# Performance work log

Measured on AMD Instinct MI355X. Metric: run time of the kernel, lower is better.

Reference implementation:

```python
import jax, jax.numpy as jnp
import numpy as np

B, S, H, I, G = 4, 2048, 2048, 8192, 128


def _onebit_quant(w, group_size):
    # Group-wise 1-bit (sign) quantization along the input dim with per-group
    # abs-mean scale, as in BitNet-style OneBitLinear.
    out_f, in_f = w.shape
    wg = w.reshape(out_f, in_f // group_size, group_size)
    scale = jnp.mean(jnp.abs(wg), axis=-1, keepdims=True)  # [out, n_groups, 1]
    wq = jnp.sign(wg) * scale
    return wq.reshape(out_f, in_f)


def setup_inputs() -> dict:
    key = jax.random.key(0)
    k1, k2, k3, k4 = jax.random.split(key, 4)
    return {
        "x": jax.random.normal(k1, (B, S, H), dtype=jnp.float32),
        "w_gate": jax.random.normal(k2, (I, H), dtype=jnp.float32) * 0.02,
        "w_up": jax.random.normal(k3, (I, H), dtype=jnp.float32) * 0.02,
        "w_down": jax.random.normal(k4, (H, I), dtype=jnp.float32) * 0.02,
        "group_size": G,
    }


def reference(x, w_gate, w_up, w_down, group_size):
    wg_q = _onebit_quant(w_gate, group_size)   # [I, H]
    wu_q = _onebit_quant(w_up, group_size)     # [I, H]
    wd_q = _onebit_quant(w_down, group_size)   # [H, I]
    gate = jnp.einsum('bsh,ih->bsi', x, wg_q)  # [B, S, I]
    up = jnp.einsum('bsh,ih->bsi', x, wu_q)    # [B, S, I]
    h = jax.nn.silu(gate) * up                 # [B, S, I]
    return jnp.einsum('bsi,hi->bsh', h, wd_q)  # [B, S, H]
```

## Files before the change

kernel.cpp:

```cpp
#include <hip/hip_runtime.h>
#include <hip/hip_bf16.h>
#include <cstdint>
#include <cstddef>

using bf16 = __hip_bfloat16;

typedef __attribute__((ext_vector_type(8))) short short8;
typedef __attribute__((ext_vector_type(4))) float f32x4;
typedef __attribute__((ext_vector_type(4))) unsigned short us4;

static constexpr int Bb = 4, Ss = 2048, Hh = 2048, Ii = 8192, Gg = 128;
static constexpr int Mm = Bb * Ss;

#define MEMFENCE() asm volatile("" ::: "memory")
#define BARRIER() do { MEMFENCE(); __builtin_amdgcn_s_barrier(); MEMFENCE(); } while (0)

__global__ void quant_onebit(const float* __restrict__ w, bf16* __restrict__ wq,
                             int ngroups) {
  int gid = blockIdx.x * 4 + (threadIdx.x >> 6);
  if (gid >= ngroups) return;
  int lane = threadIdx.x & 63;
  size_t base = (size_t)gid * Gg + (size_t)lane * 2;
  float2 v = *(const float2*)(w + base);
  float s = fabsf(v.x) + fabsf(v.y);
#pragma unroll
  for (int m = 32; m >= 1; m >>= 1) s += __shfl_xor(s, m);
  float scale = s * (1.0f / 128.0f);
  float q0 = (v.x > 0.f) ? scale : ((v.x < 0.f) ? -scale : 0.f);
  float q1 = (v.y > 0.f) ? scale : ((v.y < 0.f) ? -scale : 0.f);
  unsigned int p =
      (unsigned int)__builtin_bit_cast(unsigned short, __float2bfloat16(q0)) |
      ((unsigned int)__builtin_bit_cast(unsigned short, __float2bfloat16(q1)) << 16);
  *(unsigned int*)(wq + base) = p;
}

__global__ void cast_f32_bf16(const float* __restrict__ in, bf16* __restrict__ out,
                              size_t n4) {
  size_t i = (size_t)blockIdx.x * blockDim.x + threadIdx.x;
  if (i >= n4) return;
  float4 v = *(const float4*)(in + i * 4);
  us4 o;
  o.x = __builtin_bit_cast(unsigned short, __float2bfloat16(v.x));
  o.y = __builtin_bit_cast(unsigned short, __float2bfloat16(v.y));
  o.z = __builtin_bit_cast(unsigned short, __float2bfloat16(v.z));
  o.w = __builtin_bit_cast(unsigned short, __float2bfloat16(v.w));
  *(us4*)(out + i * 4) = o;
}

__device__ __forceinline__ void gload16(const bf16* g, char* l) {
  __builtin_amdgcn_global_load_lds(
      (const __attribute__((address_space(1))) void*)g,
      (__attribute__((address_space(3))) void*)l, 16, 0, 0);
}

__device__ __forceinline__ short8 lfrag(const char* part, int row, int s) {
  return *(const short8*)(part + row * 64 + (((s ^ (row >> 1)) & 3) << 4));
}

template <bool DUAL>
__global__ __launch_bounds__(512, 2)
void gemm_bt8(const bf16* __restrict__ A,
              const bf16* __restrict__ B0,
              const bf16* __restrict__ B1,
              bf16* __restrict__ OutBf,
              float* __restrict__ OutF,
              int M, int N, int K) {
  constexpr int BM = 256, BN = DUAL ? 128 : 256;
  constexpr int NF = DUAL ? 2 : 4;
  extern __shared__ char smem[];

  const int tid = threadIdx.x;
  const int wid = tid >> 6;
  const int lane = tid & 63;
  const int wr = wid >> 2;
  const int wc = wid & 3;
  const int lrow = lane & 15;
  const int ks = lane >> 4;

  const int nbx = N / BN;
  const int nbm = M / BM;
  const int nwg = (int)gridDim.x;
  const int cpx = nwg >> 3;
  const int wg = (int)blockIdx.x;
  const int L = (wg & 7) * cpx + (wg >> 3);
  constexpr int CN = 8;
  const int chunk = L / (nbm * CN);
  const int within = L % (nbm * CN);
  const int m0 = (within / CN) * BM;
  const int n0 = (chunk * CN + (within % CN)) * BN;

  const int NT = K / 32;

  const int srow = tid >> 2;
  const int slog8 = (((tid & 3) ^ ((tid >> 3) & 3)) << 3);
  const bf16* pA0 = A + (size_t)(m0 + srow) * K + slog8;
  const bf16* pA1 = pA0 + (size_t)128 * K;
  const bf16* pB0 = B0 + (size_t)(n0 + srow) * K + slog8;
  const bf16* pB1 = DUAL ? (B1 + (size_t)(n0 + srow) * K + slog8)
                         : (pB0 + (size_t)128 * K);
  const int dA = wid * 1024;

  auto stageA = [&](int t) {
    char* b = smem + (size_t)(t & 1) * 32768;
    const int koff = t * 32;
    gload16(pA0 + koff, b + dA);
    gload16(pA1 + koff, b + 8192 + dA);
  };
  auto stageB = [&](int t) {
    char* b = smem + (size_t)(t & 1) * 32768 + 16384;
    const int koff = t * 32;
    gload16(pB0 + koff, b + dA);
    gload16(pB1 + koff, b + 8192 + dA);
  };

  const f32x4 vzero = {0.f, 0.f, 0.f, 0.f};
  f32x4 acc0[8][NF];
  f32x4 acc1[DUAL ? 8 : 1][NF];
#pragma unroll
  for (int mf = 0; mf < 8; ++mf)
#pragma unroll
    for (int nf = 0; nf < NF; ++nf) {
      acc0[mf][nf] = vzero;
      if constexpr (DUAL) acc1[mf][nf] = vzero;
    }

  stageA(0); stageB(0);

  short8 fa[4], fb0[NF], fb1[DUAL ? NF : 1];

  for (int t = 0; t < NT; ++t) {
    asm volatile("s_waitcnt vmcnt(0)" ::: "memory");
    BARRIER();
    const char* Ap = smem + (size_t)(t & 1) * 32768;
    const char* Bp = Ap + 16384;

    if constexpr (DUAL) {
#pragma unroll
      for (int nf = 0; nf < 2; ++nf) {
        fb0[nf] = lfrag(Bp, wc * 32 + nf * 16 + lrow, ks);
        fb1[nf] = lfrag(Bp + 8192, wc * 32 + nf * 16 + lrow, ks);
      }
    } else {
#pragma unroll
      for (int nf = 0; nf < 4; ++nf)
        fb0[nf] = lfrag(Bp, wc * 64 + nf * 16 + lrow, ks);
    }
#pragma unroll
    for (int i = 0; i < 4; ++i)
      fa[i] = lfrag(Ap, wr * 128 + i * 16 + lrow, ks);
    if (t + 1 < NT) stageA(t + 1);
    __builtin_amdgcn_s_setprio(1);
#pragma unroll
    for (int i = 0; i < 4; ++i)
#pragma unroll
      for (int nf = 0; nf < NF; ++nf) {
        acc0[i][nf] = __builtin_amdgcn_mfma_f32_16x16x32_bf16(
            fa[i], fb0[nf], acc0[i][nf], 0, 0, 0);
        if constexpr (DUAL)
          acc1[i][nf] = __builtin_amdgcn_mfma_f32_16x16x32_bf16(
              fa[i], fb1[nf], acc1[i][nf], 0, 0, 0);
      }
    __builtin_amdgcn_s_setprio(0);
    BARRIER();

#pragma unroll
    for (int i = 0; i < 4; ++i)
      fa[i] = lfrag(Ap, wr * 128 + 64 + i * 16 + lrow, ks);
    if (t + 1 < NT) stageB(t + 1);
    __builtin_amdgcn_s_setprio(1);
#pragma unroll
    for (int i = 0; i < 4; ++i)
#pragma unroll
      for (int nf = 0; nf < NF; ++nf) {
        acc0[4 + i][nf] = __builtin_amdgcn_mfma_f32_16x16x32_bf16(
            fa[i], fb0[nf], acc0[4 + i][nf], 0, 0, 0);
        if constexpr (DUAL)
          acc1[4 + i][nf] = __builtin_amdgcn_mfma_f32_16x16x32_bf16(
              fa[i], fb1[nf], acc1[4 + i][nf], 0, 0, 0);
      }
    __builtin_amdgcn_s_setprio(0);
  }

  const int crow0 = (lane >> 4) * 4;
  const int ccol = lane & 15;
#pragma unroll
  for (int mf = 0; mf < 8; ++mf)
#pragma unroll
    for (int nf = 0; nf < NF; ++nf)
#pragma unroll
      for (int j = 0; j < 4; ++j) {
        const int row = m0 + wr * 128 + mf * 16 + crow0 + j;
        if constexpr (DUAL) {
          const int col = n0 + wc * 32 + nf * 16 + ccol;
          float g = acc0[mf][nf][j];
          float u = acc1[mf][nf][j];
          OutBf[(size_t)row * N + col] =
              __float2bfloat16(g / (1.0f + expf(-g)) * u);
        } else {
          const int col = n0 + wc * 64 + nf * 16 + ccol;
          OutF[(size_t)row * N + col] = acc0[mf][nf][j];
        }
      }
}

extern "C" void kernel_launch(void* const* d_in, const int* in_sizes, int n_in,
                              void* d_out, int out_size, void* d_ws, size_t ws_size,
                              hipStream_t stream) {
  const float* x = (const float*)d_in[0];
  const float* wg = (const float*)d_in[1];
  const float* wu = (const float*)d_in[2];
  const float* wd = (const float*)d_in[3];
  float* out = (float*)d_out;

  char* ws = (char*)d_ws;
  bf16* xq = (bf16*)(ws + 0);
  bf16* wgq = (bf16*)(ws + (size_t)33554432);
  bf16* wuq = (bf16*)(ws + (size_t)67108864);
  bf16* hbuf = (bf16*)(ws + (size_t)100663296);
  bf16* wdq = xq;

  auto* kDual = gemm_bt8<true>;
  auto* kSingle = gemm_bt8<false>;
  (void)hipFuncSetAttribute((const void*)kDual,
                            hipFuncAttributeMaxDynamicSharedMemorySize, 65536);
  (void)hipFuncSetAttribute((const void*)kSingle,
                            hipFuncAttributeMaxDynamicSharedMemorySize, 65536);

  const int ngW = (Ii * Hh) / Gg;
  quant_onebit<<<ngW / 4, 256, 0, stream>>>(wg, wgq, ngW);
  quant_onebit<<<ngW / 4, 256, 0, stream>>>(wu, wuq, ngW);

  const size_t n4 = (size_t)Mm * Hh / 4;
  cast_f32_bf16<<<(unsigned)((n4 + 255) / 256), 256, 0, stream>>>(x, xq, n4);

  kDual<<<(Mm / 256) * (Ii / 128), 512, 65536, stream>>>(
      xq, wgq, wuq, hbuf, nullptr, Mm, Ii, Hh);

  quant_onebit<<<ngW / 4, 256, 0, stream>>>(wd, wdq, ngW);

  kSingle<<<(Mm / 256) * (Hh / 256), 512, 65536, stream>>>(
      hbuf, wdq, nullptr, nullptr, out, Mm, Hh, Ii);
}
```

Measured before the change: 888.0 us.

## Load B fragments directly to registers and ring-buffer A in LDS

B-operand fragments are now read straight from global memory into registers, double-buffered one K-slice ahead, instead of being staged through shared memory. A tiles use a 4-slot LDS ring with prefetch distance two, so each K-slice needs only one barrier instead of two. The workgroup raster chunk width is also reduced. The aim is to cut LDS traffic and barrier overhead. In exchange, B is fetched redundantly by the two wave rows, which raises L2 traffic, and B load latency is hidden by only one slice of lookahead.

```diff
diff --git a/kernel.cpp b/kernel.cpp
--- a/kernel.cpp
+++ b/kernel.cpp
@@ -83,35 +83,37 @@
   const int cpx = nwg >> 3;
   const int wg = (int)blockIdx.x;
   const int L = (wg & 7) * cpx + (wg >> 3);
-  constexpr int CN = 8;
+  constexpr int CN = DUAL ? 2 : 1;
   const int chunk = L / (nbm * CN);
   const int within = L % (nbm * CN);
   const int m0 = (within / CN) * BM;
   const int n0 = (chunk * CN + (within % CN)) * BN;
 
-  const int NT = K / 32;
+  const int NS = K / 32;
 
   const int srow = tid >> 2;
   const int slog8 = (((tid & 3) ^ ((tid >> 3) & 3)) << 3);
   const bf16* pA0 = A + (size_t)(m0 + srow) * K + slog8;
   const bf16* pA1 = pA0 + (size_t)128 * K;
-  const bf16* pB0 = B0 + (size_t)(n0 + srow) * K + slog8;
-  const bf16* pB1 = DUAL ? (B1 + (size_t)(n0 + srow) * K + slog8)
-                         : (pB0 + (size_t)128 * K);
   const int dA = wid * 1024;
 
-  auto stageA = [&](int t) {
-    char* b = smem + (size_t)(t & 1) * 32768;
-    const int koff = t * 32;
+  auto stageA = [&](int s) {
+    char* b = smem + (size_t)(s & 3) * 16384;
+    const int koff = s * 32;
     gload16(pA0 + koff, b + dA);
     gload16(pA1 + koff, b + 8192 + dA);
   };
-  auto stageB = [&](int t) {
-    char* b = smem + (size_t)(t & 1) * 32768 + 16384;
-    const int koff = t * 32;
-    gload16(pB0 + koff, b + dA);
-    gload16(pB1 + koff, b + 8192 + dA);
-  };
+
+  const int nfK = 16 * K;
+  const bf16* fbp0;
+  const bf16* fbp1;
+  if constexpr (DUAL) {
+    fbp0 = B0 + (size_t)(n0 + wc * 32 + lrow) * K + ks * 8;
+    fbp1 = B1 + (size_t)(n0 + wc * 32 + lrow) * K + ks * 8;
+  } else {
+    fbp0 = B0 + (size_t)(n0 + wc * 64 + lrow) * K + ks * 8;
+    fbp1 = fbp0;
+  }
 
   const f32x4 vzero = {0.f, 0.f, 0.f, 0.f};
   f32x4 acc0[8][NF];
@@ -124,62 +126,76 @@
       if constexpr (DUAL) acc1[mf][nf] = vzero;
     }
 
-  stageA(0); stageB(0);
-
-  short8 fa[4], fb0[NF], fb1[DUAL ? NF : 1];
-
-  for (int t = 0; t < NT; ++t) {
-    asm volatile("s_waitcnt vmcnt(0)" ::: "memory");
-    BARRIER();
-    const char* Ap = smem + (size_t)(t & 1) * 32768;
-    const char* Bp = Ap + 16384;
-
-    if constexpr (DUAL) {
-#pragma unroll
-      for (int nf = 0; nf < 2; ++nf) {
-        fb0[nf] = lfrag(Bp, wc * 32 + nf * 16 + lrow, ks);
-        fb1[nf] = lfrag(Bp + 8192, wc * 32 + nf * 16 + lrow, ks);
-      }
-    } else {
-#pragma unroll
-      for (int nf = 0; nf < 4; ++nf)
-        fb0[nf] = lfrag(Bp, wc * 64 + nf * 16 + lrow, ks);
-    }
-#pragma unroll
-    for (int i = 0; i < 4; ++i)
-      fa[i] = lfrag(Ap, wr * 128 + i * 16 + lrow, ks);
-    if (t + 1 < NT) stageA(t + 1);
-    __builtin_amdgcn_s_setprio(1);
-#pragma unroll
-    for (int i = 0; i < 4; ++i)
-#pragma unroll
-      for (int nf = 0; nf < NF; ++nf) {
-        acc0[i][nf] = __builtin_amdgcn_mfma_f32_16x16x32_bf16(
-            fa[i], fb0[nf], acc0[i][nf], 0, 0, 0);
-        if constexpr (DUAL)
-          acc1[i][nf] = __builtin_amdgcn_mfma_f32_16x16x32_bf16(
-              fa[i], fb1[nf], acc1[i][nf], 0, 0, 0);
-      }
-    __builtin_amdgcn_s_setprio(0);
-    BARRIER();
-
-#pragma unroll
-    for (int i = 0; i < 4; ++i)
-      fa[i] = lfrag(Ap, wr * 128 + 64 + i * 16 + lrow, ks);
-    if (t + 1 < NT) stageB(t + 1);
-    __builtin_amdgcn_s_setprio(1);
-#pragma unroll
-    for (int i = 0; i < 4; ++i)
-#pragma unroll
-      for (int nf = 0; nf < NF; ++nf) {
-        acc0[4 + i][nf] = __builtin_amdgcn_mfma_f32_16x16x32_bf16(
-            fa[i], fb0[nf], acc0[4 + i][nf], 0, 0, 0);
-        if constexpr (DUAL)
-          acc1[4 + i][nf] = __builtin_amdgcn_mfma_f32_16x16x32_bf16(
-              fa[i], fb1[nf], acc1[4 + i][nf], 0, 0, 0);
-      }
-    __builtin_amdgcn_s_setprio(0);
+  short8 fbX[4], fbY[4], fa[4];
+
+#define LOADB(DST, S)                                                         \
+  do {                                                                        \
+    const int koff_ = (S) * 32;                                               \
+    if constexpr (DUAL) {                                                     \
+      DST[0] = *(const short8*)(fbp0 + koff_);                                \
+      DST[1] = *(const short8*)(fbp0 + nfK + koff_);                          \
+      DST[2] = *(const short8*)(fbp1 + koff_);                                \
+      DST[3] = *(const short8*)(fbp1 + nfK + koff_);                          \
+    } else {                                                                  \
+      DST[0] = *(const short8*)(fbp0 + koff_);                                \
+      DST[1] = *(const short8*)(fbp0 + nfK + koff_);                          \
+      DST[2] = *(const short8*)(fbp0 + 2 * nfK + koff_);                      \
+      DST[3] = *(const short8*)(fbp0 + 3 * nfK + koff_);                      \
+    }                                                                         \
+  } while (0)
+
+#define SLICE_BODY(S, CUR, NXT)                                               \
+  do {                                                                        \
+    const int s_ = (S);                                                       \
+    if (s_ + 1 < NS) asm volatile("s_waitcnt vmcnt(2)" ::: "memory");         \
+    else             asm volatile("s_waitcnt vmcnt(0)" ::: "memory");         \
+    BARRIER();                                                                \
+    if (s_ + 1 < NS) LOADB(NXT, s_ + 1);                                      \
+    const char* Ap_ = smem + (size_t)(s_ & 3) * 16384;                        \
+    _Pragma("unroll")                                                         \
+    for (int i = 0; i < 4; ++i)                                               \
+      fa[i] = lfrag(Ap_, wr * 128 + i * 16 + lrow, ks);                       \
+    if (s_ + 2 < NS) stageA(s_ + 2);                                          \
+    __builtin_amdgcn_s_setprio(1);                                            \
+    _Pragma("unroll")                                                         \
+    for (int i = 0; i < 4; ++i)                                               \
+      _Pragma("unroll")                                                       \
+      for (int nf = 0; nf < NF; ++nf) {                                       \
+        acc0[i][nf] = __builtin_amdgcn_mfma_f32_16x16x32_bf16(                \
+            fa[i], CUR[nf], acc0[i][nf], 0, 0, 0);                            \
+        if constexpr (DUAL)                                                   \
+          acc1[i][nf] = __builtin_amdgcn_mfma_f32_16x16x32_bf16(              \
+              fa[i], CUR[2 + nf], acc1[i][nf], 0, 0, 0);                      \
+      }                                                                       \
+    __builtin_amdgcn_s_setprio(0);                                            \
+    _Pragma("unroll")                                                         \
+    for (int i = 0; i < 4; ++i)                                               \
+      fa[i] = lfrag(Ap_, wr * 128 + 64 + i * 16 + lrow, ks);                  \
+    __builtin_amdgcn_s_setprio(1);                                            \
+    _Pragma("unroll")                                                         \
+    for (int i = 0; i < 4; ++i)                                               \
+      _Pragma("unroll")                                                       \
+      for (int nf = 0; nf < NF; ++nf) {                                       \
+        acc0[4 + i][nf] = __builtin_amdgcn_mfma_f32_16x16x32_bf16(            \
+            fa[i], CUR[nf], acc0[4 + i][nf], 0, 0, 0);                        \
+        if constexpr (DUAL)                                                   \
+          acc1[4 + i][nf] = __builtin_amdgcn_mfma_f32_16x16x32_bf16(          \
+              fa[i], CUR[2 + nf], acc1[4 + i][nf], 0, 0, 0);                  \
+      }                                                                       \
+    __builtin_amdgcn_s_setprio(0);                                            \
+  } while (0)
+
+  LOADB(fbX, 0);
+  stageA(0);
+  stageA(1);
+
+  for (int s = 0; s < NS; s += 2) {
+    SLICE_BODY(s, fbX, fbY);
+    SLICE_BODY(s + 1, fbY, fbX);
   }
+
+#undef SLICE_BODY
+#undef LOADB
 
   const int crow0 = (lane >> 4) * 4;
   const int ccol = lane & 15;
```

Result: slower. 1.244 ms (+40.0%).
